# Kernel optimization log

Hardware: AMD Instinct MI355X
Metric: run time of the kernel (lower is better)

Reference implementation:

```python
import jax, jax.numpy as jnp
import numpy as np
from jax import lax

REP_THR = 0.6
BORDER = 10


def setup_inputs() -> dict:
    key = jax.random.key(0)
    # repeatability heatmap in [0, 1), NCHW
    repeatability = jax.random.uniform(key, (16, 1, 1536, 1536), dtype=jnp.float32)
    return {"repeatability": repeatability}


def _local_max(x):
    # 3x3 stride-1 max pool with padding=1 (torch pads with -inf for maxpool)
    return lax.reduce_window(
        x, -jnp.inf, lax.max,
        window_dimensions=(1, 1, 3, 3),
        window_strides=(1, 1, 1, 1),
        padding=((0, 0), (0, 0), (1, 1), (1, 1)),
    )


def reference(repeatability):
    B, C, H, W = repeatability.shape
    maxima = (repeatability == _local_max(repeatability)) & (repeatability >= REP_THR)
    # border mask: zero out a 10-pixel frame
    border = jnp.zeros((H, W), dtype=bool).at[BORDER:-BORDER, BORDER:-BORDER].set(True)
    maxima = maxima & border  # broadcasts over (B, C)
    # nonzero().t()[2:4] -> row/col (y, x) coordinates of surviving maxima, shape [2, K]
    idx = jnp.nonzero(maxima)  # tuple (b, c, y, x); dynamic-shaped, eager only
    return jnp.stack(idx)[2:4]
```

## Files before the change

### kernel.cpp

```cpp
#include <hip/hip_runtime.h>

#define W 1536
#define H 1536
#define NB 16
#define NROWS (NB * H)
#define SH 24
#define NBLK (NROWS / SH)
#define BLOCK1 384
#define CPR 24
#define NMASK (NROWS * CPR)
#define BLOCK2 (SH * CPR)
#define NW2 (BLOCK2 / 64)
#define CAP 5376
#define REP_THR 0.6f

__device__ __forceinline__ float max3f(float a, float b, float c) {
    return fmaxf(fmaxf(a, b), c);
}

__global__ __launch_bounds__(BLOCK1) void nms_pass1(const float* __restrict__ in,
                                                    unsigned long long* __restrict__ masks,
                                                    unsigned int* __restrict__ counts) {
    const int t = threadIdx.x;
    const int lane = t & 63;
    const int wv = t >> 6;
    const int blk = blockIdx.x;
    const int r0 = blk * SH;
    const int ytile = blk % (H / SH);

    const int c0 = 4 * t;
    const int cl = (t == 0) ? 0 : c0 - 1;
    const int cr = (t == BLOCK1 - 1) ? (W - 1) : c0 + 4;

    unsigned colm = 0xFu;
    if (t <= 1) colm = 0u;
    else if (t == 2) colm = 0xCu;
    if (t >= 382) colm = 0u;
    else if (t == 381) colm = 0x3u;

    auto rowp = [&](int i) {
        int ir = r0 - 1 + i;
        ir = ir < 0 ? 0 : (ir >= NROWS ? NROWS - 1 : ir);
        return in + (size_t)ir * W;
    };

    auto mkhalo = [&](float4 v, float lw, float rx) {
        float lw_all = __shfl_up(v.w, 1, 64);
        if (lane == 0) lw_all = lw;
        float rx_all = __shfl_down(v.x, 1, 64);
        if (lane == 63) rx_all = rx;
        float4 h;
        h.x = max3f(lw_all, v.x, v.y);
        h.y = max3f(v.x, v.y, v.z);
        h.z = max3f(v.y, v.z, v.w);
        h.w = max3f(v.z, v.w, rx_all);
        return h;
    };

    float4 v0 = *(const float4*)(rowp(0) + c0);
    float lw0 = 0.f, rx0 = 0.f;
    if (lane == 0) lw0 = rowp(0)[cl];
    if (lane == 63) rx0 = rowp(0)[cr];
    float4 v1 = *(const float4*)(rowp(1) + c0);
    float lw1 = 0.f, rx1 = 0.f;
    if (lane == 0) lw1 = rowp(1)[cl];
    if (lane == 63) rx1 = rowp(1)[cr];
    float4 vN = *(const float4*)(rowp(2) + c0);
    float lwN = 0.f, rxN = 0.f;
    if (lane == 0) lwN = rowp(2)[cl];
    if (lane == 63) rxN = rowp(2)[cr];

    float4 hA = mkhalo(v0, lw0, rx0);
    float4 hB = mkhalo(v1, lw1, rx1);
    float4 ctrB = v1;

    unsigned cnt = 0;
#pragma unroll
    for (int i = 2; i <= SH + 1; ++i) {
        float4 v = vN;
        float lwc = lwN, rxc = rxN;
        vN = *(const float4*)(rowp(i + 1) + c0);
        lwN = 0.f; rxN = 0.f;
        if (lane == 0) lwN = rowp(i + 1)[cl];
        if (lane == 63) rxN = rowp(i + 1)[cr];

        float4 hC = mkhalo(v, lwc, rxc);

        const int yloc = ytile * SH + (i - 2);
        unsigned nib = 0u;
        if (yloc >= 10 && yloc < H - 10) {
            nib |= (ctrB.x >= fmaxf(max3f(hA.x, hB.x, hC.x), REP_THR)) ? 1u : 0u;
            nib |= (ctrB.y >= fmaxf(max3f(hA.y, hB.y, hC.y), REP_THR)) ? 2u : 0u;
            nib |= (ctrB.z >= fmaxf(max3f(hA.z, hB.z, hC.z), REP_THR)) ? 4u : 0u;
            nib |= (ctrB.w >= fmaxf(max3f(hA.w, hB.w, hC.w), REP_THR)) ? 8u : 0u;
            nib &= colm;
        }
        cnt += __popc(nib);
        unsigned x = nib;
        x |= __shfl_down(x, 1, 64) << 4;
        x |= __shfl_down(x, 2, 64) << 8;
        x |= __shfl_down(x, 4, 64) << 16;
        unsigned hi = __shfl_down(x, 8, 64);
        if ((lane & 15) == 0) {
            unsigned long long m64 = (unsigned long long)x | ((unsigned long long)hi << 32);
            masks[(size_t)(r0 + i - 2) * CPR + (t >> 4)] = m64;
        }
        hA = hB; hB = hC; ctrB = v;
    }

#pragma unroll
    for (int o = 32; o > 0; o >>= 1) cnt += __shfl_down(cnt, o, 64);
    __shared__ unsigned wsum[BLOCK1 / 64];
    if (lane == 0) wsum[wv] = cnt;
    __syncthreads();
    if (t == 0) {
        unsigned s = 0;
#pragma unroll
        for (int k = 0; k < BLOCK1 / 64; ++k) s += wsum[k];
        counts[blk] = s;
    }
}

__global__ __launch_bounds__(BLOCK2) void nms_scatter(const unsigned long long* __restrict__ masks,
                                                      const unsigned int* __restrict__ counts,
                                                      int* __restrict__ out, unsigned int K) {
    __shared__ unsigned wtot[NW2];
    __shared__ unsigned sred[NW2];
    __shared__ unsigned pk[CAP];
    const int t = threadIdx.x, lane = t & 63, wv = t >> 6;
    const int blk = blockIdx.x;
    unsigned long long bits = masks[(size_t)blk * BLOCK2 + t];
    const unsigned cnt = (unsigned)__popcll(bits);
    unsigned incl = cnt;
#pragma unroll
    for (int o = 1; o < 64; o <<= 1) {
        unsigned u = __shfl_up(incl, o, 64);
        if (lane >= o) incl += u;
    }
    unsigned part = 0;
    if (t < blk) part += counts[t];
    if (t + BLOCK2 < blk) part += counts[t + BLOCK2];
#pragma unroll
    for (int o = 32; o > 0; o >>= 1) part += __shfl_down(part, o, 64);
    if (lane == 63) wtot[wv] = incl;
    if (lane == 0) sred[wv] = part;
    __syncthreads();
    unsigned blockBase = 0, blockCnt = 0, wbase = 0;
#pragma unroll
    for (int k = 0; k < NW2; ++k) {
        blockBase += sred[k];
        blockCnt += wtot[k];
        if (k < wv) wbase += wtot[k];
    }
    unsigned local = wbase + (incl - cnt);
    if (bits) {
        const int y = (blk % (H / SH)) * SH + t / CPR;
        const int x0 = (t % CPR) * 64;
        while (bits) {
            int j = __builtin_ctzll(bits);
            bits &= bits - 1ull;
            if (local < CAP) {
                pk[local] = (unsigned)y | ((unsigned)(x0 + j) << 16);
            } else {
                unsigned g = blockBase + local;
                if (g < K) { out[g] = y; out[K + g] = x0 + j; }
            }
            ++local;
        }
    }
    __syncthreads();
    const unsigned lim = blockCnt < CAP ? blockCnt : CAP;
    for (unsigned i = t; i < lim; i += BLOCK2) {
        unsigned g = blockBase + i;
        if (g < K) {
            unsigned p = pk[i];
            out[g] = (int)(p & 0xFFFFu);
            out[K + g] = (int)(p >> 16);
        }
    }
}

extern "C" void kernel_launch(void* const* d_in, const int* in_sizes, int n_in,
                              void* d_out, int out_size, void* d_ws, size_t ws_size,
                              hipStream_t stream) {
    const float* in = (const float*)d_in[0];
    int* out = (int*)d_out;
    unsigned long long* masks = (unsigned long long*)d_ws;
    unsigned int* counts = (unsigned int*)((char*)d_ws + (size_t)NMASK * 8);
    const unsigned K = (unsigned)(out_size / 2);

    nms_pass1<<<NBLK, BLOCK1, 0, stream>>>(in, masks, counts);
    nms_scatter<<<NBLK, BLOCK2, 0, stream>>>(masks, counts, out, K);
}
```

Measured before the change: 247.0 us.

## Fuse mask and scatter kernels into one pass with decoupled look-back scan

```diff
diff --git a/kernel.cpp b/kernel.cpp
--- a/kernel.cpp
+++ b/kernel.cpp
@@ -4,33 +4,41 @@
 #define H 1536
 #define NB 16
 #define NROWS (NB * H)
-#define SH 24
-#define NBLK (NROWS / SH)
-#define BLOCK1 384
+#define SH 16
+#define NTILE (NROWS / SH)
+#define BLOCK 384
 #define CPR 24
-#define NMASK (NROWS * CPR)
-#define BLOCK2 (SH * CPR)
-#define NW2 (BLOCK2 / 64)
-#define CAP 5376
+#define CHUNKS (SH * CPR)
+#define NW (BLOCK / 64)
+#define CAP 4096
 #define REP_THR 0.6f
+#define FLAG_PARTIAL   (1ull << 62)
+#define FLAG_INCLUSIVE (2ull << 62)
 
 __device__ __forceinline__ float max3f(float a, float b, float c) {
     return fmaxf(fmaxf(a, b), c);
 }
 
-__global__ __launch_bounds__(BLOCK1) void nms_pass1(const float* __restrict__ in,
-                                                    unsigned long long* __restrict__ masks,
-                                                    unsigned int* __restrict__ counts) {
-    const int t = threadIdx.x;
-    const int lane = t & 63;
-    const int wv = t >> 6;
-    const int blk = blockIdx.x;
-    const int r0 = blk * SH;
-    const int ytile = blk % (H / SH);
+__global__ __launch_bounds__(BLOCK) void nms_onepass(const float* __restrict__ in,
+                                                     unsigned int* __restrict__ ticket,
+                                                     unsigned long long* __restrict__ status,
+                                                     int* __restrict__ out,
+                                                     unsigned int K) {
+    __shared__ unsigned long long lmask[CHUNKS];
+    __shared__ unsigned wtot[NW];
+    __shared__ unsigned pk[CAP];
+    __shared__ unsigned sTile, sBase;
+
+    const int t = threadIdx.x, lane = t & 63, wv = t >> 6;
+    if (t == 0) sTile = atomicAdd(ticket, 1u);
+    __syncthreads();
+    const int tile = (int)sTile;
+    const int r0 = tile * SH;
+    const int ytile = tile % (H / SH);
 
     const int c0 = 4 * t;
     const int cl = (t == 0) ? 0 : c0 - 1;
-    const int cr = (t == BLOCK1 - 1) ? (W - 1) : c0 + 4;
+    const int cr = (t == BLOCK - 1) ? (W - 1) : c0 + 4;
 
     unsigned colm = 0xFu;
     if (t <= 1) colm = 0u;
@@ -74,7 +82,6 @@
     float4 hB = mkhalo(v1, lw1, rx1);
     float4 ctrB = v1;
 
-    unsigned cnt = 0;
 #pragma unroll
     for (int i = 2; i <= SH + 1; ++i) {
         float4 v = vN;
@@ -95,7 +102,6 @@
             nib |= (ctrB.w >= fmaxf(max3f(hA.w, hB.w, hC.w), REP_THR)) ? 8u : 0u;
             nib &= colm;
         }
-        cnt += __popc(nib);
         unsigned x = nib;
         x |= __shfl_down(x, 1, 64) << 4;
         x |= __shfl_down(x, 2, 64) << 8;
@@ -103,33 +109,13 @@
         unsigned hi = __shfl_down(x, 8, 64);
         if ((lane & 15) == 0) {
             unsigned long long m64 = (unsigned long long)x | ((unsigned long long)hi << 32);
-            masks[(size_t)(r0 + i - 2) * CPR + (t >> 4)] = m64;
+            lmask[(i - 2) * CPR + (t >> 4)] = m64;
         }
         hA = hB; hB = hC; ctrB = v;
     }
-
-#pragma unroll
-    for (int o = 32; o > 0; o >>= 1) cnt += __shfl_down(cnt, o, 64);
-    __shared__ unsigned wsum[BLOCK1 / 64];
-    if (lane == 0) wsum[wv] = cnt;
-    __syncthreads();
-    if (t == 0) {
-        unsigned s = 0;
-#pragma unroll
-        for (int k = 0; k < BLOCK1 / 64; ++k) s += wsum[k];
-        counts[blk] = s;
-    }
-}
-
-__global__ __launch_bounds__(BLOCK2) void nms_scatter(const unsigned long long* __restrict__ masks,
-                                                      const unsigned int* __restrict__ counts,
-                                                      int* __restrict__ out, unsigned int K) {
-    __shared__ unsigned wtot[NW2];
-    __shared__ unsigned sred[NW2];
-    __shared__ unsigned pk[CAP];
-    const int t = threadIdx.x, lane = t & 63, wv = t >> 6;
-    const int blk = blockIdx.x;
-    unsigned long long bits = masks[(size_t)blk * BLOCK2 + t];
+    __syncthreads();
+
+    unsigned long long bits = lmask[t];
     const unsigned cnt = (unsigned)__popcll(bits);
     unsigned incl = cnt;
 #pragma unroll
@@ -137,24 +123,65 @@
         unsigned u = __shfl_up(incl, o, 64);
         if (lane >= o) incl += u;
     }
-    unsigned part = 0;
-    if (t < blk) part += counts[t];
-    if (t + BLOCK2 < blk) part += counts[t + BLOCK2];
-#pragma unroll
-    for (int o = 32; o > 0; o >>= 1) part += __shfl_down(part, o, 64);
     if (lane == 63) wtot[wv] = incl;
-    if (lane == 0) sred[wv] = part;
-    __syncthreads();
-    unsigned blockBase = 0, blockCnt = 0, wbase = 0;
-#pragma unroll
-    for (int k = 0; k < NW2; ++k) {
-        blockBase += sred[k];
+    __syncthreads();
+
+    if (wv == 0) {
+        unsigned agg = 0;
+#pragma unroll
+        for (int k = 0; k < NW; ++k) agg += wtot[k];
+        if (lane == 0 && tile > 0)
+            __hip_atomic_store(&status[tile], FLAG_PARTIAL | (unsigned long long)agg,
+                               __ATOMIC_RELEASE, __HIP_MEMORY_SCOPE_AGENT);
+        unsigned long long excl = 0;
+        int idx = tile - 1;
+        while (idx >= 0) {
+            const int src = idx - lane;
+            unsigned long long s;
+            if (src >= 0) {
+                do {
+                    s = __hip_atomic_load(&status[src], __ATOMIC_ACQUIRE,
+                                          __HIP_MEMORY_SCOPE_AGENT);
+                } while (!(s >> 62));
+            } else {
+                s = FLAG_INCLUSIVE;
+            }
+            const unsigned long long val = s & 0xFFFFFFFFull;
+            const unsigned long long ball = __ballot((s >> 62) == 2ull);
+            if (ball) {
+                const int li = __ffsll((unsigned long long)ball) - 1;
+                unsigned long long contrib = (lane <= li) ? val : 0ull;
+#pragma unroll
+                for (int o = 32; o > 0; o >>= 1) contrib += __shfl_down(contrib, o, 64);
+                excl += __shfl(contrib, 0, 64);
+                break;
+            } else {
+                unsigned long long contrib = val;
+#pragma unroll
+                for (int o = 32; o > 0; o >>= 1) contrib += __shfl_down(contrib, o, 64);
+                excl += __shfl(contrib, 0, 64);
+                idx -= 64;
+            }
+        }
+        if (lane == 0) {
+            __hip_atomic_store(&status[tile],
+                               FLAG_INCLUSIVE | (excl + (unsigned long long)agg),
+                               __ATOMIC_RELEASE, __HIP_MEMORY_SCOPE_AGENT);
+            sBase = (unsigned)excl;
+        }
+    }
+    __syncthreads();
+
+    const unsigned blockBase = sBase;
+    unsigned blockCnt = 0, wbase = 0;
+#pragma unroll
+    for (int k = 0; k < NW; ++k) {
         blockCnt += wtot[k];
         if (k < wv) wbase += wtot[k];
     }
     unsigned local = wbase + (incl - cnt);
     if (bits) {
-        const int y = (blk % (H / SH)) * SH + t / CPR;
+        const int y = ytile * SH + t / CPR;
         const int x0 = (t % CPR) * 64;
         while (bits) {
             int j = __builtin_ctzll(bits);
@@ -170,7 +197,7 @@
     }
     __syncthreads();
     const unsigned lim = blockCnt < CAP ? blockCnt : CAP;
-    for (unsigned i = t; i < lim; i += BLOCK2) {
+    for (unsigned i = t; i < lim; i += BLOCK) {
         unsigned g = blockBase + i;
         if (g < K) {
             unsigned p = pk[i];
@@ -185,10 +212,10 @@
                               hipStream_t stream) {
     const float* in = (const float*)d_in[0];
     int* out = (int*)d_out;
-    unsigned long long* masks = (unsigned long long*)d_ws;
-    unsigned int* counts = (unsigned int*)((char*)d_ws + (size_t)NMASK * 8);
+    unsigned int* ticket = (unsigned int*)d_ws;
+    unsigned long long* status = (unsigned long long*)((char*)d_ws + 8);
     const unsigned K = (unsigned)(out_size / 2);
 
-    nms_pass1<<<NBLK, BLOCK1, 0, stream>>>(in, masks, counts);
-    nms_scatter<<<NBLK, BLOCK2, 0, stream>>>(masks, counts, out, K);
+    hipMemsetAsync(d_ws, 0, 8 + (size_t)NTILE * 8, stream);
+    nms_onepass<<<NTILE, BLOCK, 0, stream>>>(in, ticket, status, out, K);
 }
```

Result: slower. 403.8 us (+63.5%).
